# Performance work log

Hardware: AMD Instinct MI355X
Metric: run time of the kernel (lower is better)

Reference implementation:

```python
import jax, jax.numpy as jnp
import numpy as np

N_HEAD = 16

def setup_inputs() -> dict:
    key = jax.random.key(0)
    ks = jax.random.split(key, 4)
    C = 2048
    x = jax.random.normal(ks[0], (4, 2048, C), dtype=jnp.float32)
    # weights stored [in, out] (transpose of torch Linear's [out, in]); same math y = x @ W + b
    w_qkv = jax.random.normal(ks[1], (C, 3 * C), dtype=jnp.float32) * (1.0 / np.sqrt(C))
    b_qkv = jnp.zeros((3 * C,), dtype=jnp.float32)
    w_proj = jax.random.normal(ks[2], (C, C), dtype=jnp.float32) * (1.0 / np.sqrt(C))
    b_proj = jnp.zeros((C,), dtype=jnp.float32)
    return {"x": x, "w_qkv": w_qkv, "b_qkv": b_qkv, "w_proj": w_proj, "b_proj": b_proj}

def reference(x, w_qkv, b_qkv, w_proj, b_proj):
    B, S, C = x.shape
    H = N_HEAD
    D = C // H
    qkv = x @ w_qkv + b_qkv                      # [B,S,3C]
    q, k, v = jnp.split(qkv, 3, axis=-1)
    # [B,H,S,D]
    q = q.reshape(B, S, H, D).transpose(0, 2, 1, 3)
    k = k.reshape(B, S, H, D).transpose(0, 2, 1, 3)
    v = v.reshape(B, S, H, D).transpose(0, 2, 1, 3)
    scale = 1.0 / np.sqrt(D).astype(np.float32)
    scores = jnp.einsum('bhqd,bhkd->bhqk', q, k) * scale   # [B,H,S,S]
    causal = jnp.tril(jnp.ones((S, S), dtype=bool))
    scores = jnp.where(causal, scores, jnp.finfo(scores.dtype).min)
    attn = jax.nn.softmax(scores, axis=-1)
    y = jnp.einsum('bhqk,bhkd->bhqd', attn, v)              # [B,H,S,D]
    y = y.transpose(0, 2, 1, 3).reshape(B, S, C)
    return y @ w_proj + b_proj
```

## Files before the change

### kernel.cpp

```cpp
#include <hip/hip_runtime.h>
#include <hip/hip_bf16.h>

typedef __bf16 bf16x8 __attribute__((ext_vector_type(8)));
typedef float floatx4 __attribute__((ext_vector_type(4)));

__device__ __forceinline__ unsigned short f2bf(float f) {
  unsigned u = __float_as_uint(f);
  u += 0x7fffu + ((u >> 16) & 1u);
  return (unsigned short)(u >> 16);
}

__device__ __forceinline__ unsigned cvt_pk_bf16(float lo, float hi) {
  unsigned r;
  asm("v_cvt_pk_bf16_f32 %0, %1, %2" : "=v"(r) : "v"(lo), "v"(hi));
  return r;
}

__device__ __forceinline__ void async_copy16(const void* g, void* l) {
  __builtin_amdgcn_global_load_lds(
      (const __attribute__((address_space(1))) void*)g,
      (__attribute__((address_space(3))) void*)l, 16, 0, 0);
}

__global__ __launch_bounds__(256) void cvt_bf16(
    const float* __restrict__ in, unsigned short* __restrict__ out) {
  size_t i = ((size_t)blockIdx.x * 256 + threadIdx.x) * 8;
  float4 a0 = *(const float4*)&in[i];
  float4 a1 = *(const float4*)&in[i + 4];
  uint4 d;
  d.x = (unsigned)f2bf(a0.x) | ((unsigned)f2bf(a0.y) << 16);
  d.y = (unsigned)f2bf(a0.z) | ((unsigned)f2bf(a0.w) << 16);
  d.z = (unsigned)f2bf(a1.x) | ((unsigned)f2bf(a1.y) << 16);
  d.w = (unsigned)f2bf(a1.z) | ((unsigned)f2bf(a1.w) << 16);
  *(uint4*)(&out[i]) = d;
}

__global__ __launch_bounds__(256) void transpose_cvt(
    const float* __restrict__ in, unsigned short* __restrict__ out,
    int R, int Ccol) {
  __shared__ unsigned short tile[32][33];
  int c0 = blockIdx.x * 32, r0 = blockIdx.y * 32;
  int tx = threadIdx.x & 31, ty = threadIdx.x >> 5;
  #pragma unroll
  for (int i = 0; i < 32; i += 8)
    tile[ty + i][tx] = f2bf(in[(size_t)(r0 + ty + i) * Ccol + c0 + tx]);
  __syncthreads();
  #pragma unroll
  for (int i = 0; i < 32; i += 8)
    out[(size_t)(c0 + ty + i) * R + r0 + tx] = tile[tx][ty + i];
}

__device__ __forceinline__ void gemm_bt_mainloop(
    const unsigned short* __restrict__ A, const unsigned short* __restrict__ Bt,
    int K, int m0, int n0,
    unsigned short* As, unsigned short* Bs, floatx4 acc[4][4]) {
  const int t = threadIdx.x;
  const int lane = t & 63, w = t >> 6;
  const int wm = w >> 1, wn = w & 1;
  const int l15 = lane & 15, l4 = lane >> 4;
  const int lrow = lane >> 3, lchunk = lane & 7;
  const int gch = lchunk ^ lrow;
  const floatx4 zf = {0.f, 0.f, 0.f, 0.f};
  #pragma unroll
  for (int mi = 0; mi < 4; mi++)
    #pragma unroll
    for (int ni = 0; ni < 4; ni++) acc[mi][ni] = zf;

  for (int k0 = 0; k0 < K; k0 += 64) {
    __syncthreads();
    #pragma unroll
    for (int i = 0; i < 4; i++) {
      int ridx = w * 4 + i;
      int row = ridx * 8 + lrow;
      async_copy16(&A[(size_t)(m0 + row) * K + k0 + gch * 8], &As[ridx * 512]);
    }
    #pragma unroll
    for (int i = 0; i < 4; i++) {
      int ridx = w * 4 + i;
      int row = ridx * 8 + lrow;
      async_copy16(&Bt[(size_t)(n0 + row) * K + k0 + gch * 8], &Bs[ridx * 512]);
    }
    __syncthreads();
    #pragma unroll
    for (int kk = 0; kk < 2; kk++) {
      bf16x8 af[4], bfr[4];
      #pragma unroll
      for (int mi = 0; mi < 4; mi++) {
        int row = wm * 64 + mi * 16 + l15;
        af[mi] = *(const bf16x8*)(&As[row * 64 + ((kk * 4 + l4) ^ (l15 & 7)) * 8]);
      }
      #pragma unroll
      for (int ni = 0; ni < 4; ni++) {
        int row = wn * 64 + ni * 16 + l15;
        bfr[ni] = *(const bf16x8*)(&Bs[row * 64 + ((kk * 4 + l4) ^ (l15 & 7)) * 8]);
      }
      #pragma unroll
      for (int mi = 0; mi < 4; mi++)
        #pragma unroll
        for (int ni = 0; ni < 4; ni++)
          acc[mi][ni] = __builtin_amdgcn_mfma_f32_16x16x32_bf16(
              af[mi], bfr[ni], acc[mi][ni], 0, 0, 0);
    }
  }
}

__global__ __launch_bounds__(256, 3) void gemm_qkv(
    const unsigned short* __restrict__ X, const unsigned short* __restrict__ WT,
    const float* __restrict__ bias,
    unsigned short* __restrict__ Qo, unsigned short* __restrict__ Ko,
    unsigned short* __restrict__ Vto) {
  __shared__ unsigned short As[128 * 64];
  __shared__ unsigned short Bs[128 * 64];
  int n0 = blockIdx.x * 128, m0 = blockIdx.y * 128;
  floatx4 acc[4][4];
  gemm_bt_mainloop(X, WT, 2048, m0, n0, As, Bs, acc);

  const int t = threadIdx.x, lane = t & 63, w = t >> 6;
  const int wm = w >> 1, wn = w & 1;
  const int l15 = lane & 15, l4 = lane >> 4;
  int which = n0 >> 11;
  int h = (n0 & 2047) >> 7;
  int b = m0 >> 11;
  int s0 = m0 & 2047;
  float bv[4];
  #pragma unroll
  for (int ni = 0; ni < 4; ni++)
    bv[ni] = bias[n0 + wn * 64 + ni * 16 + l15];

  if (which < 2) {
    unsigned short* dst = (which == 0) ? Qo : Ko;
    size_t base = (size_t)(b * 16 + h) * 2048;
    #pragma unroll
    for (int mi = 0; mi < 4; mi++)
      #pragma unroll
      for (int ni = 0; ni < 4; ni++) {
        int d = wn * 64 + ni * 16 + l15;
        #pragma unroll
        for (int r = 0; r < 4; r++) {
          int srow = s0 + wm * 64 + mi * 16 + l4 * 4 + r;
          dst[(base + srow) * 128 + d] = f2bf(acc[mi][ni][r] + bv[ni]);
        }
      }
  } else {
    #pragma unroll
    for (int mi = 0; mi < 4; mi++)
      #pragma unroll
      for (int ni = 0; ni < 4; ni++) {
        int d = wn * 64 + ni * 16 + l15;
        int sr = s0 + wm * 64 + mi * 16 + l4 * 4;
        ushort4 v;
        v.x = f2bf(acc[mi][ni][0] + bv[ni]);
        v.y = f2bf(acc[mi][ni][1] + bv[ni]);
        v.z = f2bf(acc[mi][ni][2] + bv[ni]);
        v.w = f2bf(acc[mi][ni][3] + bv[ni]);
        *(ushort4*)(&Vto[((size_t)(b * 16 + h) * 128 + d) * 2048 + sr]) = v;
      }
  }
}

__device__ __forceinline__ void attn_stage(
    const unsigned short* __restrict__ Kb, const unsigned short* __restrict__ Vb,
    __bf16* Ksel, __bf16* Vsel, int k0, int lane, int w) {
  const int krow_in = lane >> 4, kch = lane & 15;
  const int vrow_in = lane >> 3, vch = lane & 7;
  #pragma unroll
  for (int u = 0; u < 2; u++) {
    int uk = w * 2 + u;
    int row = uk * 4 + krow_in;
    int sch = kch ^ (row & 7);
    async_copy16(&Kb[(size_t)(k0 + row) * 128 + sch * 8], Ksel + uk * 512);
  }
  #pragma unroll
  for (int u = 0; u < 2; u++) {
    int uv = w * 2 + u;
    int row = uv * 8 + vrow_in;
    int sch = vch ^ vrow_in;
    async_copy16(&Vb[(size_t)row * 2048 + k0 + sch * 8], Vsel + uv * 512);
  }
}

__global__ __launch_bounds__(512, 4) void attn(
    const unsigned short* __restrict__ Qg, const unsigned short* __restrict__ Kg,
    const unsigned short* __restrict__ Vtg, unsigned short* __restrict__ Yg) {
  const int S = 2048, Dh = 128;
  const float c1 = 0.08838834764831845f * 1.4426950408889634f;
  const float NEG_BIG = -3.0e38f;
  __shared__ __bf16 Ks[2][64 * 128];
  __shared__ __bf16 Vs[2][128 * 64];
  __shared__ __bf16 Ps[8][16 * 64];

  int wg = blockIdx.x;
  int lg = (wg & 7) * 64 + (wg >> 3);
  int qtp = lg & 7;
  int bh = lg >> 3;
  const int t = threadIdx.x, lane = t & 63, w = t >> 6;
  const int l15 = lane & 15, l4 = lane >> 4;
  const unsigned short* Qb = Qg + (size_t)bh * S * Dh;
  const unsigned short* Kb = Kg + (size_t)bh * S * Dh;
  const unsigned short* Vb = Vtg + (size_t)bh * Dh * S;
  __bf16* Pw = Ps[w];
  int b = bh >> 4, h = bh & 15;
  const floatx4 zf = {0.f, 0.f, 0.f, 0.f};

  #pragma unroll 1
  for (int half = 0; half < 2; half++) {
    int jq = half ? qtp : (15 - qtp);
    int qb0 = jq * 128;
    int qrow_base = qb0 + w * 16;
    bf16x8 qf[4];
    #pragma unroll
    for (int kk = 0; kk < 4; kk++)
      qf[kk] = *(const bf16x8*)(
          &Qb[(size_t)(qrow_base + l15) * Dh + kk * 32 + l4 * 8]);
    floatx4 accO[8];
    #pragma unroll
    for (int nd = 0; nd < 8; nd++) accO[nd] = zf;
    float mst = NEG_BIG, lst = 0.f;

    int ntiles = 2 * jq + 2;
    int cur = 0;
    attn_stage(Kb, Vb, Ks[0], Vs[0], 0, lane, w);
    __syncthreads();

    #pragma unroll 1
    for (int kt = 0; kt < ntiles; kt++) {
      if (kt + 1 < ntiles)
        attn_stage(Kb, Vb, Ks[cur ^ 1], Vs[cur ^ 1], (kt + 1) * 64, lane, w);

      const __bf16* Kcur = Ks[cur];
      const __bf16* Vcur = Vs[cur];
      floatx4 sc[4];
      #pragma unroll
      for (int ni = 0; ni < 4; ni++) sc[ni] = zf;
      __builtin_amdgcn_s_setprio(1);
      #pragma unroll
      for (int kk = 0; kk < 4; kk++) {
        bf16x8 kf[4];
        #pragma unroll
        for (int ni = 0; ni < 4; ni++) {
          int row = ni * 16 + l15;
          kf[ni] = *(const bf16x8*)(
              &Kcur[row * 128 + (((kk * 4 + l4) ^ (l15 & 7)) << 3)]);
        }
        #pragma unroll
        for (int ni = 0; ni < 4; ni++)
          sc[ni] = __builtin_amdgcn_mfma_f32_16x16x32_bf16(kf[ni], qf[kk], sc[ni], 0, 0, 0);
      }
      __builtin_amdgcn_s_setprio(0);

      if (kt >= 2 * jq) {
        int kb = kt * 64 - qb0 - w * 16 - l15;
        #pragma unroll
        for (int ni = 0; ni < 4; ni++)
          #pragma unroll
          for (int r = 0; r < 4; r++)
            if (kb + ni * 16 + l4 * 4 + r > 0) sc[ni][r] = NEG_BIG;
      }

      float mt = fmaxf(fmaxf(fmaxf(sc[0][0], sc[0][1]), fmaxf(sc[0][2], sc[0][3])),
                       fmaxf(fmaxf(sc[1][0], sc[1][1]), fmaxf(sc[1][2], sc[1][3])));
      mt = fmaxf(mt,
           fmaxf(fmaxf(fmaxf(sc[2][0], sc[2][1]), fmaxf(sc[2][2], sc[2][3])),
                 fmaxf(fmaxf(sc[3][0], sc[3][1]), fmaxf(sc[3][2], sc[3][3]))));
      mt = fmaxf(mt, __shfl_xor(mt, 16, 64));
      mt = fmaxf(mt, __shfl_xor(mt, 32, 64));

      if (!__all(mt <= mst + 8.0f)) {
        float mnew = fmaxf(mst, mt);
        float alpha = exp2f((mst - mnew) * c1);
        mst = mnew;
        lst *= alpha;
        float ar[4];
        #pragma unroll
        for (int r = 0; r < 4; r++)
          ar[r] = __shfl(alpha, l4 * 20 + r, 64);
        #pragma unroll
        for (int nd = 0; nd < 8; nd++)
          #pragma unroll
          for (int r = 0; r < 4; r++) accO[nd][r] *= ar[r];
      }

      float mc = mst * c1;
      float p[4][4];
      float rs = 0.f;
      #pragma unroll
      for (int ni = 0; ni < 4; ni++)
        #pragma unroll
        for (int r = 0; r < 4; r++) {
          p[ni][r] = exp2f(sc[ni][r] * c1 - mc);
          rs += p[ni][r];
        }
      rs += __shfl_xor(rs, 16, 64);
      rs += __shfl_xor(rs, 32, 64);
      lst += rs;

      #pragma unroll
      for (int ni = 0; ni < 4; ni++) {
        uint2 dw;
        dw.x = cvt_pk_bf16(p[ni][0], p[ni][1]);
        dw.y = cvt_pk_bf16(p[ni][2], p[ni][3]);
        int s = ni * 4 + l4;
        *(uint2*)(&Pw[l15 * 64 + (((s >> 1) ^ (l15 & 7)) << 3) + ((s & 1) << 2)]) = dw;
      }

      __builtin_amdgcn_s_setprio(1);
      #pragma unroll
      for (int kk = 0; kk < 2; kk++) {
        bf16x8 pf = *(const bf16x8*)(
            &Pw[l15 * 64 + (((kk * 4 + l4) ^ (l15 & 7)) << 3)]);
        #pragma unroll
        for (int nd = 0; nd < 8; nd++) {
          int row = nd * 16 + l15;
          bf16x8 vf = *(const bf16x8*)(
              &Vcur[row * 64 + (((kk * 4 + l4) ^ (l15 & 7)) << 3)]);
          accO[nd] = __builtin_amdgcn_mfma_f32_16x16x32_bf16(pf, vf, accO[nd], 0, 0, 0);
        }
      }
      __builtin_amdgcn_s_setprio(0);
      __syncthreads();
      cur ^= 1;
    }

    float invl = 1.0f / lst;
    float ivr[4];
    #pragma unroll
    for (int r = 0; r < 4; r++)
      ivr[r] = __shfl(invl, l4 * 20 + r, 64);
    #pragma unroll
    for (int r = 0; r < 4; r++) {
      int srow = qrow_base + l4 * 4 + r;
      size_t rowbase = ((size_t)(b * 2048 + srow)) * 2048 + h * 128;
      #pragma unroll
      for (int nd = 0; nd < 8; nd++)
        Yg[rowbase + nd * 16 + l15] = f2bf(accO[nd][r] * ivr[r]);
    }
  }
}

__global__ __launch_bounds__(256, 3) void gemm_proj(
    const unsigned short* __restrict__ Yin, const unsigned short* __restrict__ WT,
    const float* __restrict__ bias, float* __restrict__ Og) {
  __shared__ unsigned short As[128 * 64];
  __shared__ unsigned short Bs[128 * 64];
  int n0 = blockIdx.x * 128, m0 = blockIdx.y * 128;
  floatx4 acc[4][4];
  gemm_bt_mainloop(Yin, WT, 2048, m0, n0, As, Bs, acc);

  const int t = threadIdx.x, lane = t & 63, w = t >> 6;
  const int wm = w >> 1, wn = w & 1;
  const int l15 = lane & 15, l4 = lane >> 4;
  float bv[4];
  #pragma unroll
  for (int ni = 0; ni < 4; ni++)
    bv[ni] = bias[n0 + wn * 64 + ni * 16 + l15];
  #pragma unroll
  for (int mi = 0; mi < 4; mi++)
    #pragma unroll
    for (int ni = 0; ni < 4; ni++)
      #pragma unroll
      for (int r = 0; r < 4; r++)
        Og[(size_t)(m0 + wm * 64 + mi * 16 + l4 * 4 + r) * 2048 +
           n0 + wn * 64 + ni * 16 + l15] = acc[mi][ni][r] + bv[ni];
}

extern "C" void kernel_launch(void* const* d_in, const int* in_sizes, int n_in,
                              void* d_out, int out_size, void* d_ws, size_t ws_size,
                              hipStream_t stream) {
  const float* x      = (const float*)d_in[0];
  const float* w_qkv  = (const float*)d_in[1];
  const float* b_qkv  = (const float*)d_in[2];
  const float* w_proj = (const float*)d_in[3];
  const float* b_proj = (const float*)d_in[4];
  float* out = (float*)d_out;
  char* ws = (char*)d_ws;

  unsigned short* Q   = (unsigned short*)d_out;
  unsigned short* Kt  = (unsigned short*)((char*)d_out + 33554432);
  unsigned short* Vt  = (unsigned short*)(ws);
  unsigned short* Xbf = (unsigned short*)(ws + 33554432);
  unsigned short* Y   = (unsigned short*)(ws + 33554432);
  unsigned short* WqT = (unsigned short*)(ws + 67108864);
  unsigned short* WpT = (unsigned short*)(ws + 67108864);

  cvt_bf16<<<dim3(8192), 256, 0, stream>>>(x, Xbf);
  transpose_cvt<<<dim3(192, 64), 256, 0, stream>>>(w_qkv, WqT, 2048, 6144);
  gemm_qkv<<<dim3(48, 64), 256, 0, stream>>>(Xbf, WqT, b_qkv, Q, Kt, Vt);
  attn<<<dim3(512), 512, 0, stream>>>(Q, Kt, Vt, Y);
  transpose_cvt<<<dim3(64, 64), 256, 0, stream>>>(w_proj, WpT, 2048, 2048);
  gemm_proj<<<dim3(16, 64), 256, 0, stream>>>(Y, WpT, b_proj, out);
}
```

Baseline: 565.2 us.

## Use 256x256 double-buffered GEMM tiles with XCD-aware block remapping

Both GEMMs move from 128x128 tiles with 4 waves to 256x256 tiles with 8 waves, raising arithmetic intensity per LDS load. The k-loop becomes double-buffered: the next tile is staged while the current one is computed, with barriers and setprio around the MFMA bursts. The grid becomes 1D and blocks are remapped so neighbouring tiles land on the same XCD, for L2 reuse. The cost is 128KB of LDS and 128 accumulator floats per thread, which limits occupancy and adds register pressure. The smaller grids (768 and 256 blocks) may also underfill the CUs.

```diff
diff --git a/kernel.cpp b/kernel.cpp
--- a/kernel.cpp
+++ b/kernel.cpp
@@ -50,104 +50,139 @@
     out[(size_t)(c0 + ty + i) * R + r0 + tx] = tile[tx][ty + i];
 }
 
-__device__ __forceinline__ void gemm_bt_mainloop(
+__device__ __forceinline__ void stage_tile256(
+    const unsigned short* __restrict__ A, const unsigned short* __restrict__ Bt,
+    int K, int m0, int n0, int k0,
+    unsigned short* As, unsigned short* Bs, int lane, int w) {
+  const int lrow = lane >> 3;
+  const int gch = (lane & 7) ^ lrow;
+  #pragma unroll
+  for (int u = 0; u < 4; u++) {
+    int g = w * 4 + u;
+    int row = g * 8 + lrow;
+    async_copy16(&A[(size_t)(m0 + row) * K + k0 + gch * 8], &As[g * 512]);
+  }
+  #pragma unroll
+  for (int u = 0; u < 4; u++) {
+    int g = w * 4 + u;
+    int row = g * 8 + lrow;
+    async_copy16(&Bt[(size_t)(n0 + row) * K + k0 + gch * 8], &Bs[g * 512]);
+  }
+}
+
+__device__ __forceinline__ void gemm_bt_256(
     const unsigned short* __restrict__ A, const unsigned short* __restrict__ Bt,
     int K, int m0, int n0,
-    unsigned short* As, unsigned short* Bs, floatx4 acc[4][4]) {
-  const int t = threadIdx.x;
-  const int lane = t & 63, w = t >> 6;
-  const int wm = w >> 1, wn = w & 1;
+    unsigned short* AsB, unsigned short* BsB,
+    floatx4 acc[8][4]) {
+  const int t = threadIdx.x, lane = t & 63, w = t >> 6;
+  const int wr = w >> 2, wc = w & 3;
   const int l15 = lane & 15, l4 = lane >> 4;
-  const int lrow = lane >> 3, lchunk = lane & 7;
-  const int gch = lchunk ^ lrow;
   const floatx4 zf = {0.f, 0.f, 0.f, 0.f};
   #pragma unroll
-  for (int mi = 0; mi < 4; mi++)
+  for (int mi = 0; mi < 8; mi++)
     #pragma unroll
     for (int ni = 0; ni < 4; ni++) acc[mi][ni] = zf;
 
-  for (int k0 = 0; k0 < K; k0 += 64) {
-    __syncthreads();
-    #pragma unroll
-    for (int i = 0; i < 4; i++) {
-      int ridx = w * 4 + i;
-      int row = ridx * 8 + lrow;
-      async_copy16(&A[(size_t)(m0 + row) * K + k0 + gch * 8], &As[ridx * 512]);
-    }
-    #pragma unroll
-    for (int i = 0; i < 4; i++) {
-      int ridx = w * 4 + i;
-      int row = ridx * 8 + lrow;
-      async_copy16(&Bt[(size_t)(n0 + row) * K + k0 + gch * 8], &Bs[ridx * 512]);
+  const int nkt = K >> 6;
+  stage_tile256(A, Bt, K, m0, n0, 0, AsB, BsB, lane, w);
+  __syncthreads();
+
+  #pragma unroll 1
+  for (int kt = 0; kt < nkt; kt++) {
+    const unsigned short* Ab = AsB + (kt & 1) * 16384;
+    const unsigned short* Bb = BsB + (kt & 1) * 16384;
+    if (kt + 1 < nkt)
+      stage_tile256(A, Bt, K, m0, n0, (kt + 1) * 64,
+                    AsB + ((kt + 1) & 1) * 16384,
+                    BsB + ((kt + 1) & 1) * 16384, lane, w);
+    #pragma unroll
+    for (int j = 0; j < 4; j++) {
+      const int qm = j >> 1, qn = j & 1;
+      bf16x8 af[4][2], bfr[2][2];
+      #pragma unroll
+      for (int mi = 0; mi < 4; mi++) {
+        int row = wr * 128 + (qm * 4 + mi) * 16 + l15;
+        #pragma unroll
+        for (int kk = 0; kk < 2; kk++)
+          af[mi][kk] = *(const bf16x8*)(
+              &Ab[row * 64 + (((kk * 4 + l4) ^ (l15 & 7)) << 3)]);
+      }
+      #pragma unroll
+      for (int ni = 0; ni < 2; ni++) {
+        int row = wc * 64 + (qn * 2 + ni) * 16 + l15;
+        #pragma unroll
+        for (int kk = 0; kk < 2; kk++)
+          bfr[ni][kk] = *(const bf16x8*)(
+              &Bb[row * 64 + (((kk * 4 + l4) ^ (l15 & 7)) << 3)]);
+      }
+      __builtin_amdgcn_s_barrier();
+      __builtin_amdgcn_s_setprio(1);
+      #pragma unroll
+      for (int kk = 0; kk < 2; kk++)
+        #pragma unroll
+        for (int mi = 0; mi < 4; mi++)
+          #pragma unroll
+          for (int ni = 0; ni < 2; ni++)
+            acc[qm * 4 + mi][qn * 2 + ni] = __builtin_amdgcn_mfma_f32_16x16x32_bf16(
+                af[mi][kk], bfr[ni][kk], acc[qm * 4 + mi][qn * 2 + ni], 0, 0, 0);
+      __builtin_amdgcn_s_setprio(0);
+      if (j < 3) __builtin_amdgcn_s_barrier();
     }
     __syncthreads();
-    #pragma unroll
-    for (int kk = 0; kk < 2; kk++) {
-      bf16x8 af[4], bfr[4];
-      #pragma unroll
-      for (int mi = 0; mi < 4; mi++) {
-        int row = wm * 64 + mi * 16 + l15;
-        af[mi] = *(const bf16x8*)(&As[row * 64 + ((kk * 4 + l4) ^ (l15 & 7)) * 8]);
-      }
-      #pragma unroll
-      for (int ni = 0; ni < 4; ni++) {
-        int row = wn * 64 + ni * 16 + l15;
-        bfr[ni] = *(const bf16x8*)(&Bs[row * 64 + ((kk * 4 + l4) ^ (l15 & 7)) * 8]);
-      }
-      #pragma unroll
-      for (int mi = 0; mi < 4; mi++)
-        #pragma unroll
-        for (int ni = 0; ni < 4; ni++)
-          acc[mi][ni] = __builtin_amdgcn_mfma_f32_16x16x32_bf16(
-              af[mi], bfr[ni], acc[mi][ni], 0, 0, 0);
-    }
-  }
-}
-
-__global__ __launch_bounds__(256, 3) void gemm_qkv(
+  }
+}
+
+__global__ __launch_bounds__(512, 2) void gemm_qkv(
     const unsigned short* __restrict__ X, const unsigned short* __restrict__ WT,
     const float* __restrict__ bias,
     unsigned short* __restrict__ Qo, unsigned short* __restrict__ Ko,
     unsigned short* __restrict__ Vto) {
-  __shared__ unsigned short As[128 * 64];
-  __shared__ unsigned short Bs[128 * 64];
-  int n0 = blockIdx.x * 128, m0 = blockIdx.y * 128;
-  floatx4 acc[4][4];
-  gemm_bt_mainloop(X, WT, 2048, m0, n0, As, Bs, acc);
+  __shared__ unsigned short As[2][256 * 64];
+  __shared__ unsigned short Bs[2][256 * 64];
+  int id = blockIdx.x;
+  int n8 = gridDim.x >> 3;
+  int lg = (id & 7) * n8 + (id >> 3);
+  int bm = lg & 31, bn = lg >> 5;
+  int m0 = bm * 256, n0 = bn * 256;
+  floatx4 acc[8][4];
+  gemm_bt_256(X, WT, 2048, m0, n0, As[0], Bs[0], acc);
 
   const int t = threadIdx.x, lane = t & 63, w = t >> 6;
-  const int wm = w >> 1, wn = w & 1;
+  const int wr = w >> 2, wc = w & 3;
   const int l15 = lane & 15, l4 = lane >> 4;
   int which = n0 >> 11;
-  int h = (n0 & 2047) >> 7;
   int b = m0 >> 11;
   int s0 = m0 & 2047;
   float bv[4];
   #pragma unroll
   for (int ni = 0; ni < 4; ni++)
-    bv[ni] = bias[n0 + wn * 64 + ni * 16 + l15];
+    bv[ni] = bias[n0 + wc * 64 + ni * 16 + l15];
 
   if (which < 2) {
     unsigned short* dst = (which == 0) ? Qo : Ko;
-    size_t base = (size_t)(b * 16 + h) * 2048;
-    #pragma unroll
-    for (int mi = 0; mi < 4; mi++)
-      #pragma unroll
-      for (int ni = 0; ni < 4; ni++) {
-        int d = wn * 64 + ni * 16 + l15;
+    #pragma unroll
+    for (int ni = 0; ni < 4; ni++) {
+      int cn = (n0 & 2047) + wc * 64 + ni * 16;
+      int h = cn >> 7, d = (cn & 127) + l15;
+      size_t base = ((size_t)(b * 16 + h)) * 2048;
+      #pragma unroll
+      for (int mi = 0; mi < 8; mi++) {
         #pragma unroll
         for (int r = 0; r < 4; r++) {
-          int srow = s0 + wm * 64 + mi * 16 + l4 * 4 + r;
+          int srow = s0 + wr * 128 + mi * 16 + l4 * 4 + r;
           dst[(base + srow) * 128 + d] = f2bf(acc[mi][ni][r] + bv[ni]);
         }
       }
+    }
   } else {
     #pragma unroll
-    for (int mi = 0; mi < 4; mi++)
-      #pragma unroll
-      for (int ni = 0; ni < 4; ni++) {
-        int d = wn * 64 + ni * 16 + l15;
-        int sr = s0 + wm * 64 + mi * 16 + l4 * 4;
+    for (int ni = 0; ni < 4; ni++) {
+      int cn = (n0 & 2047) + wc * 64 + ni * 16;
+      int h = cn >> 7, d = (cn & 127) + l15;
+      #pragma unroll
+      for (int mi = 0; mi < 8; mi++) {
+        int sr = s0 + wr * 128 + mi * 16 + l4 * 4;
         ushort4 v;
         v.x = f2bf(acc[mi][ni][0] + bv[ni]);
         v.y = f2bf(acc[mi][ni][1] + bv[ni]);
@@ -155,6 +190,7 @@
         v.w = f2bf(acc[mi][ni][3] + bv[ni]);
         *(ushort4*)(&Vto[((size_t)(b * 16 + h) * 128 + d) * 2048 + sr]) = v;
       }
+    }
   }
 }
 
@@ -337,30 +373,34 @@
   }
 }
 
-__global__ __launch_bounds__(256, 3) void gemm_proj(
+__global__ __launch_bounds__(512, 2) void gemm_proj(
     const unsigned short* __restrict__ Yin, const unsigned short* __restrict__ WT,
     const float* __restrict__ bias, float* __restrict__ Og) {
-  __shared__ unsigned short As[128 * 64];
-  __shared__ unsigned short Bs[128 * 64];
-  int n0 = blockIdx.x * 128, m0 = blockIdx.y * 128;
-  floatx4 acc[4][4];
-  gemm_bt_mainloop(Yin, WT, 2048, m0, n0, As, Bs, acc);
+  __shared__ unsigned short As[2][256 * 64];
+  __shared__ unsigned short Bs[2][256 * 64];
+  int id = blockIdx.x;
+  int n8 = gridDim.x >> 3;
+  int lg = (id & 7) * n8 + (id >> 3);
+  int bm = lg & 31, bn = lg >> 5;
+  int m0 = bm * 256, n0 = bn * 256;
+  floatx4 acc[8][4];
+  gemm_bt_256(Yin, WT, 2048, m0, n0, As[0], Bs[0], acc);
 
   const int t = threadIdx.x, lane = t & 63, w = t >> 6;
-  const int wm = w >> 1, wn = w & 1;
+  const int wr = w >> 2, wc = w & 3;
   const int l15 = lane & 15, l4 = lane >> 4;
   float bv[4];
   #pragma unroll
   for (int ni = 0; ni < 4; ni++)
-    bv[ni] = bias[n0 + wn * 64 + ni * 16 + l15];
-  #pragma unroll
-  for (int mi = 0; mi < 4; mi++)
+    bv[ni] = bias[n0 + wc * 64 + ni * 16 + l15];
+  #pragma unroll
+  for (int mi = 0; mi < 8; mi++)
     #pragma unroll
     for (int ni = 0; ni < 4; ni++)
       #pragma unroll
       for (int r = 0; r < 4; r++)
-        Og[(size_t)(m0 + wm * 64 + mi * 16 + l4 * 4 + r) * 2048 +
-           n0 + wn * 64 + ni * 16 + l15] = acc[mi][ni][r] + bv[ni];
+        Og[(size_t)(m0 + wr * 128 + mi * 16 + l4 * 4 + r) * 2048 +
+           n0 + wc * 64 + ni * 16 + l15] = acc[mi][ni][r] + bv[ni];
 }
 
 extern "C" void kernel_launch(void* const* d_in, const int* in_sizes, int n_in,
@@ -384,8 +424,8 @@
 
   cvt_bf16<<<dim3(8192), 256, 0, stream>>>(x, Xbf);
   transpose_cvt<<<dim3(192, 64), 256, 0, stream>>>(w_qkv, WqT, 2048, 6144);
-  gemm_qkv<<<dim3(48, 64), 256, 0, stream>>>(Xbf, WqT, b_qkv, Q, Kt, Vt);
+  gemm_qkv<<<dim3(768), 512, 0, stream>>>(Xbf, WqT, b_qkv, Q, Kt, Vt);
   attn<<<dim3(512), 512, 0, stream>>>(Q, Kt, Vt, Y);
   transpose_cvt<<<dim3(64, 64), 256, 0, stream>>>(w_proj, WpT, 2048, 2048);
-  gemm_proj<<<dim3(16, 64), 256, 0, stream>>>(Y, WpT, b_proj, out);
-}
+  gemm_proj<<<dim3(256), 512, 0, stream>>>(Y, WpT, b_proj, out);
+}
```

Measured after the change: 681.6 us. 20.6% more time.
